# Kernel tuning notes

Measured on AMD Instinct MI355X. Metric: run time of the kernel, lower is better.

The kernel has to match this reference:

```python
import jax, jax.numpy as jnp
import numpy as np

B, S, DK = 32, 2048, 64

def setup_inputs() -> dict:
    key = jax.random.key(0)
    kq, kk, kv = jax.random.split(key, 3)
    Q = jax.random.normal(kq, (B, S, DK), dtype=jnp.float32)
    K = jax.random.normal(kk, (B, S, DK), dtype=jnp.float32)
    V = jax.random.normal(kv, (B, S, DK), dtype=jnp.float32)
    return {"Q": Q, "K": K, "V": V}

def reference(Q, K, V):
    # attn_scores = Q K^T / sqrt(d_k); full [B,S,S] probs materialized (naive, non-flash)
    d_k = Q.shape[-1]
    scores = jnp.einsum('bqd,bkd->bqk', Q, K) / jnp.sqrt(jnp.asarray(d_k, Q.dtype))
    probs = jax.nn.softmax(scores, axis=-1)
    return jnp.einsum('bqk,bkd->bqd', probs, V)
```

## Files before the change

### kernel.cpp

```cpp
#include <hip/hip_runtime.h>
#include <hip/hip_bf16.h>

#define BATCH 32
#define SEQ   2048
#define DKK   64

constexpr int QT  = 128;
constexpr int KT  = 64;
constexpr int NIT = SEQ / KT;
constexpr int LST = 66;

typedef __attribute__((ext_vector_type(8)))  short bf16x8;
typedef __attribute__((ext_vector_type(16))) float f32x16;
typedef __attribute__((ext_vector_type(2)))  unsigned uint2v;

__device__ __forceinline__ unsigned cvt2(float a, float b) {
    union { __hip_bfloat162 h; unsigned u; } c;
    c.h = __float22bfloat162_rn(make_float2(a, b));
    return c.u;
}

__device__ __forceinline__ float fast_exp2(float x) {
#if __has_builtin(__builtin_amdgcn_exp2f)
    return __builtin_amdgcn_exp2f(x);
#else
    return exp2f(x);
#endif
}

__global__ __launch_bounds__(256, 2) void attn_fwd(
        const float* __restrict__ Q, const float* __restrict__ K,
        const float* __restrict__ V, float* __restrict__ O) {
    __shared__ short Kb[2][KT][LST];
    __shared__ short Vt[2][DKK][LST];

    const int tid  = threadIdx.x;
    const int w    = tid >> 6;
    const int lane = tid & 63;
    const int hi   = lane >> 5;
    const int l31  = lane & 31;

    const int lin  = (int)blockIdx.x + ((int)blockIdx.y << 4);
    const int work = ((lin & 7) << 6) | (lin >> 3);
    const int b    = work >> 4;
    const int q0   = (work & 15) * QT + w * 32;

    const float qscale = 0.125f * 1.44269504088896340736f;
    bf16x8 qfrag[4];
    #pragma unroll
    for (int c = 0; c < 4; ++c) {
        const float* qp = Q + ((size_t)b * SEQ + q0 + l31) * DKK + 16*c + 8*hi;
        float4 a  = *(const float4*)qp;
        float4 a2 = *(const float4*)(qp + 4);
        union { bf16x8 v; unsigned u[4]; } f;
        f.u[0] = cvt2(a.x*qscale,  a.y*qscale);
        f.u[1] = cvt2(a.z*qscale,  a.w*qscale);
        f.u[2] = cvt2(a2.x*qscale, a2.y*qscale);
        f.u[3] = cvt2(a2.z*qscale, a2.w*qscale);
        qfrag[c] = f.v;
    }

    f32x16 o0 = {}, o1 = {};
    float lsum = 0.f;

    const float* Kbase = K + (size_t)b * SEQ * DKK;
    const float* Vbase = V + (size_t)b * SEQ * DKK;

    const int krow0 = tid >> 4;
    const int kcol  = (tid & 15) << 2;
    const int vd    = tid & 63;
    const int vg    = (tid >> 6) << 4;

    float4 kp[4];
    float  vp[16];
    auto load_regs = [&](int t) {
        const float* Kg = Kbase + (size_t)(t * KT) * DKK;
        #pragma unroll
        for (int i = 0; i < 4; ++i)
            kp[i] = *(const float4*)(Kg + (size_t)(krow0 + 16*i) * DKK + kcol);
        const float* Vg = Vbase + (size_t)(t * KT + vg) * DKK + vd;
        #pragma unroll
        for (int i = 0; i < 16; ++i) vp[i] = Vg[(size_t)i * DKK];
    };
    auto write_lds = [&](int buf) {
        #pragma unroll
        for (int i = 0; i < 4; ++i) {
            int2 kk;
            kk.x = (int)cvt2(kp[i].x, kp[i].y);
            kk.y = (int)cvt2(kp[i].z, kp[i].w);
            *(int2*)&Kb[buf][krow0 + 16*i][kcol] = kk;
        }
        union { bf16x8 v; unsigned u[4]; } t0, t1;
        t0.u[0] = cvt2(vp[0],  vp[1]);  t0.u[1] = cvt2(vp[2],  vp[3]);
        t0.u[2] = cvt2(vp[4],  vp[5]);  t0.u[3] = cvt2(vp[6],  vp[7]);
        t1.u[0] = cvt2(vp[8],  vp[9]);  t1.u[1] = cvt2(vp[10], vp[11]);
        t1.u[2] = cvt2(vp[12], vp[13]); t1.u[3] = cvt2(vp[14], vp[15]);
        *(bf16x8*)&Vt[buf][vd][vg]     = t0.v;
        *(bf16x8*)&Vt[buf][vd][vg + 8] = t1.v;
    };

    load_regs(0);
    write_lds(0);
    load_regs(1);
    __syncthreads();

    for (int it = 0; it < NIT; ++it) {
        const int cur = it & 1;

        #pragma unroll
        for (int kt2 = 0; kt2 < 2; ++kt2) {
            f32x16 acc = {};
            #pragma unroll
            for (int c = 0; c < 4; ++c) {
                bf16x8 kf = *(const bf16x8*)&Kb[cur][32*kt2 + l31][16*c + 8*hi];
                acc = __builtin_amdgcn_mfma_f32_32x32x16_bf16(kf, qfrag[c], acc, 0, 0, 0);
            }
            float p[16];
            #pragma unroll
            for (int r = 0; r < 16; ++r) { p[r] = fast_exp2(acc[r]); lsum += p[r]; }

            unsigned pw0 = cvt2(p[0],  p[1]),  pw1 = cvt2(p[2],  p[3]);
            unsigned pw2 = cvt2(p[4],  p[5]),  pw3 = cvt2(p[6],  p[7]);
            unsigned pw4 = cvt2(p[8],  p[9]),  pw5 = cvt2(p[10], p[11]);
            unsigned pw6 = cvt2(p[12], p[13]), pw7 = cvt2(p[14], p[15]);
            uint2v s02 = __builtin_amdgcn_permlane32_swap(pw0, pw2, false, false);
            uint2v s13 = __builtin_amdgcn_permlane32_swap(pw1, pw3, false, false);
            uint2v s46 = __builtin_amdgcn_permlane32_swap(pw4, pw6, false, false);
            uint2v s57 = __builtin_amdgcn_permlane32_swap(pw5, pw7, false, false);
            union { bf16x8 v; unsigned u[4]; } pa0, pa1;
            pa0.u[0] = s02[0]; pa0.u[1] = s13[0]; pa0.u[2] = s02[1]; pa0.u[3] = s13[1];
            pa1.u[0] = s46[0]; pa1.u[1] = s57[0]; pa1.u[2] = s46[1]; pa1.u[3] = s57[1];

            #pragma unroll
            for (int cc = 0; cc < 2; ++cc) {
                const int c = 2*kt2 + cc;
                bf16x8 pf  = cc ? pa1.v : pa0.v;
                bf16x8 vf0 = *(const bf16x8*)&Vt[cur][l31     ][16*c + 8*hi];
                bf16x8 vf1 = *(const bf16x8*)&Vt[cur][32 + l31][16*c + 8*hi];
                o0 = __builtin_amdgcn_mfma_f32_32x32x16_bf16(vf0, pf, o0, 0, 0, 0);
                o1 = __builtin_amdgcn_mfma_f32_32x32x16_bf16(vf1, pf, o1, 0, 0, 0);
            }
        }

        if (it + 1 < NIT) {
            write_lds(1 - cur);
            if (it + 2 < NIT) load_regs(it + 2);
            __syncthreads();
        }
    }

    float s = lsum;
    s += __shfl_xor(s, 32);
    const float inv = 1.0f / s;

    float* op = O + ((size_t)b * SEQ + q0 + l31) * DKK;
    #pragma unroll
    for (int G = 0; G < 4; ++G) {
        float4 st;
        st.x = o0[4*G + 0] * inv; st.y = o0[4*G + 1] * inv;
        st.z = o0[4*G + 2] * inv; st.w = o0[4*G + 3] * inv;
        *(float4*)(op + 8*G + 4*hi) = st;
        st.x = o1[4*G + 0] * inv; st.y = o1[4*G + 1] * inv;
        st.z = o1[4*G + 2] * inv; st.w = o1[4*G + 3] * inv;
        *(float4*)(op + 32 + 8*G + 4*hi) = st;
    }
}

extern "C" void kernel_launch(void* const* d_in, const int* in_sizes, int n_in,
                              void* d_out, int out_size, void* d_ws, size_t ws_size,
                              hipStream_t stream) {
    const float* Q = (const float*)d_in[0];
    const float* K = (const float*)d_in[1];
    const float* V = (const float*)d_in[2];
    float* O = (float*)d_out;
    dim3 grid(SEQ / QT, BATCH);
    attn_fwd<<<grid, dim3(256), 0, stream>>>(Q, K, V, O);
}
```

Measured before the change: 135.8 us.

## Process two query subtiles per wave with 128-thread blocks

Halves the block to two waves, each computing 64 query rows as two 32-row subtiles that share every K and V fragment read from LDS. Each thread loads and converts twice as much K/V per tile. MFMA sections are wrapped in s_setprio, and the sync becomes an explicit lgkmcnt wait plus raw barrier. This aims to cut LDS traffic per MFMA, at the cost of higher register pressure and fewer waves for latency hiding.

New measurement: 214.8 us. +58.1%, slower.

```diff
diff --git a/kernel.cpp b/kernel.cpp
--- a/kernel.cpp
+++ b/kernel.cpp
@@ -28,7 +28,7 @@
 #endif
 }
 
-__global__ __launch_bounds__(256, 2) void attn_fwd(
+__global__ __launch_bounds__(128, 2) void attn_fwd(
         const float* __restrict__ Q, const float* __restrict__ K,
         const float* __restrict__ V, float* __restrict__ O) {
     __shared__ short Kb[2][KT][LST];
@@ -43,25 +43,28 @@
     const int lin  = (int)blockIdx.x + ((int)blockIdx.y << 4);
     const int work = ((lin & 7) << 6) | (lin >> 3);
     const int b    = work >> 4;
-    const int q0   = (work & 15) * QT + w * 32;
+    const int qw   = (work & 15) * QT + w * 64;
 
     const float qscale = 0.125f * 1.44269504088896340736f;
-    bf16x8 qfrag[4];
+    bf16x8 qfrag[2][4];
     #pragma unroll
-    for (int c = 0; c < 4; ++c) {
-        const float* qp = Q + ((size_t)b * SEQ + q0 + l31) * DKK + 16*c + 8*hi;
-        float4 a  = *(const float4*)qp;
-        float4 a2 = *(const float4*)(qp + 4);
-        union { bf16x8 v; unsigned u[4]; } f;
-        f.u[0] = cvt2(a.x*qscale,  a.y*qscale);
-        f.u[1] = cvt2(a.z*qscale,  a.w*qscale);
-        f.u[2] = cvt2(a2.x*qscale, a2.y*qscale);
-        f.u[3] = cvt2(a2.z*qscale, a2.w*qscale);
-        qfrag[c] = f.v;
-    }
-
-    f32x16 o0 = {}, o1 = {};
-    float lsum = 0.f;
+    for (int qh = 0; qh < 2; ++qh) {
+        #pragma unroll
+        for (int c = 0; c < 4; ++c) {
+            const float* qp = Q + ((size_t)b * SEQ + qw + 32*qh + l31) * DKK + 16*c + 8*hi;
+            float4 a  = *(const float4*)qp;
+            float4 a2 = *(const float4*)(qp + 4);
+            union { bf16x8 v; unsigned u[4]; } f;
+            f.u[0] = cvt2(a.x*qscale,  a.y*qscale);
+            f.u[1] = cvt2(a.z*qscale,  a.w*qscale);
+            f.u[2] = cvt2(a2.x*qscale, a2.y*qscale);
+            f.u[3] = cvt2(a2.z*qscale, a2.w*qscale);
+            qfrag[qh][c] = f.v;
+        }
+    }
+
+    f32x16 o00 = {}, o01 = {}, o10 = {}, o11 = {};
+    float lsumA = 0.f, lsumB = 0.f;
 
     const float* Kbase = K + (size_t)b * SEQ * DKK;
     const float* Vbase = V + (size_t)b * SEQ * DKK;
@@ -69,34 +72,43 @@
     const int krow0 = tid >> 4;
     const int kcol  = (tid & 15) << 2;
     const int vd    = tid & 63;
-    const int vg    = (tid >> 6) << 4;
-
-    float4 kp[4];
-    float  vp[16];
+    const int vh    = tid >> 6;
+
+    float4 kp[8];
+    float  vp[32];
     auto load_regs = [&](int t) {
         const float* Kg = Kbase + (size_t)(t * KT) * DKK;
         #pragma unroll
-        for (int i = 0; i < 4; ++i)
-            kp[i] = *(const float4*)(Kg + (size_t)(krow0 + 16*i) * DKK + kcol);
-        const float* Vg = Vbase + (size_t)(t * KT + vg) * DKK + vd;
-        #pragma unroll
-        for (int i = 0; i < 16; ++i) vp[i] = Vg[(size_t)i * DKK];
+        for (int i = 0; i < 8; ++i)
+            kp[i] = *(const float4*)(Kg + (size_t)(krow0 + 8*i) * DKK + kcol);
+        const float* Vg = Vbase + (size_t)(t * KT + 16*vh) * DKK + vd;
+        #pragma unroll
+        for (int i = 0; i < 16; ++i) vp[i]      = Vg[(size_t)i * DKK];
+        const float* Vg2 = Vg + (size_t)32 * DKK;
+        #pragma unroll
+        for (int i = 0; i < 16; ++i) vp[16 + i] = Vg2[(size_t)i * DKK];
     };
     auto write_lds = [&](int buf) {
         #pragma unroll
-        for (int i = 0; i < 4; ++i) {
+        for (int i = 0; i < 8; ++i) {
             int2 kk;
             kk.x = (int)cvt2(kp[i].x, kp[i].y);
             kk.y = (int)cvt2(kp[i].z, kp[i].w);
-            *(int2*)&Kb[buf][krow0 + 16*i][kcol] = kk;
-        }
-        union { bf16x8 v; unsigned u[4]; } t0, t1;
+            *(int2*)&Kb[buf][krow0 + 8*i][kcol] = kk;
+        }
+        union { bf16x8 v; unsigned u[4]; } t0, t1, t2, t3;
         t0.u[0] = cvt2(vp[0],  vp[1]);  t0.u[1] = cvt2(vp[2],  vp[3]);
         t0.u[2] = cvt2(vp[4],  vp[5]);  t0.u[3] = cvt2(vp[6],  vp[7]);
         t1.u[0] = cvt2(vp[8],  vp[9]);  t1.u[1] = cvt2(vp[10], vp[11]);
         t1.u[2] = cvt2(vp[12], vp[13]); t1.u[3] = cvt2(vp[14], vp[15]);
-        *(bf16x8*)&Vt[buf][vd][vg]     = t0.v;
-        *(bf16x8*)&Vt[buf][vd][vg + 8] = t1.v;
+        t2.u[0] = cvt2(vp[16], vp[17]); t2.u[1] = cvt2(vp[18], vp[19]);
+        t2.u[2] = cvt2(vp[20], vp[21]); t2.u[3] = cvt2(vp[22], vp[23]);
+        t3.u[0] = cvt2(vp[24], vp[25]); t3.u[1] = cvt2(vp[26], vp[27]);
+        t3.u[2] = cvt2(vp[28], vp[29]); t3.u[3] = cvt2(vp[30], vp[31]);
+        *(bf16x8*)&Vt[buf][vd][16*vh]          = t0.v;
+        *(bf16x8*)&Vt[buf][vd][16*vh + 8]      = t1.v;
+        *(bf16x8*)&Vt[buf][vd][32 + 16*vh]     = t2.v;
+        *(bf16x8*)&Vt[buf][vd][32 + 16*vh + 8] = t3.v;
     };
 
     load_regs(0);
@@ -109,60 +121,104 @@
 
         #pragma unroll
         for (int kt2 = 0; kt2 < 2; ++kt2) {
-            f32x16 acc = {};
+            f32x16 aA = {}, aB = {};
+            __builtin_amdgcn_s_setprio(1);
             #pragma unroll
             for (int c = 0; c < 4; ++c) {
                 bf16x8 kf = *(const bf16x8*)&Kb[cur][32*kt2 + l31][16*c + 8*hi];
-                acc = __builtin_amdgcn_mfma_f32_32x32x16_bf16(kf, qfrag[c], acc, 0, 0, 0);
-            }
-            float p[16];
-            #pragma unroll
-            for (int r = 0; r < 16; ++r) { p[r] = fast_exp2(acc[r]); lsum += p[r]; }
-
-            unsigned pw0 = cvt2(p[0],  p[1]),  pw1 = cvt2(p[2],  p[3]);
-            unsigned pw2 = cvt2(p[4],  p[5]),  pw3 = cvt2(p[6],  p[7]);
-            unsigned pw4 = cvt2(p[8],  p[9]),  pw5 = cvt2(p[10], p[11]);
-            unsigned pw6 = cvt2(p[12], p[13]), pw7 = cvt2(p[14], p[15]);
-            uint2v s02 = __builtin_amdgcn_permlane32_swap(pw0, pw2, false, false);
-            uint2v s13 = __builtin_amdgcn_permlane32_swap(pw1, pw3, false, false);
-            uint2v s46 = __builtin_amdgcn_permlane32_swap(pw4, pw6, false, false);
-            uint2v s57 = __builtin_amdgcn_permlane32_swap(pw5, pw7, false, false);
-            union { bf16x8 v; unsigned u[4]; } pa0, pa1;
-            pa0.u[0] = s02[0]; pa0.u[1] = s13[0]; pa0.u[2] = s02[1]; pa0.u[3] = s13[1];
-            pa1.u[0] = s46[0]; pa1.u[1] = s57[0]; pa1.u[2] = s46[1]; pa1.u[3] = s57[1];
-
+                aA = __builtin_amdgcn_mfma_f32_32x32x16_bf16(kf, qfrag[0][c], aA, 0, 0, 0);
+                aB = __builtin_amdgcn_mfma_f32_32x32x16_bf16(kf, qfrag[1][c], aB, 0, 0, 0);
+            }
+            __builtin_amdgcn_s_setprio(0);
+
+            bf16x8 paA[2], paB[2];
+            {
+                float p[16];
+                #pragma unroll
+                for (int r = 0; r < 16; ++r) { p[r] = fast_exp2(aA[r]); lsumA += p[r]; }
+                unsigned pw0 = cvt2(p[0],  p[1]),  pw1 = cvt2(p[2],  p[3]);
+                unsigned pw2 = cvt2(p[4],  p[5]),  pw3 = cvt2(p[6],  p[7]);
+                unsigned pw4 = cvt2(p[8],  p[9]),  pw5 = cvt2(p[10], p[11]);
+                unsigned pw6 = cvt2(p[12], p[13]), pw7 = cvt2(p[14], p[15]);
+                uint2v s02 = __builtin_amdgcn_permlane32_swap(pw0, pw2, false, false);
+                uint2v s13 = __builtin_amdgcn_permlane32_swap(pw1, pw3, false, false);
+                uint2v s46 = __builtin_amdgcn_permlane32_swap(pw4, pw6, false, false);
+                uint2v s57 = __builtin_amdgcn_permlane32_swap(pw5, pw7, false, false);
+                union { bf16x8 v; unsigned u[4]; } pa0, pa1;
+                pa0.u[0] = s02[0]; pa0.u[1] = s13[0]; pa0.u[2] = s02[1]; pa0.u[3] = s13[1];
+                pa1.u[0] = s46[0]; pa1.u[1] = s57[0]; pa1.u[2] = s46[1]; pa1.u[3] = s57[1];
+                paA[0] = pa0.v; paA[1] = pa1.v;
+            }
+            {
+                float p[16];
+                #pragma unroll
+                for (int r = 0; r < 16; ++r) { p[r] = fast_exp2(aB[r]); lsumB += p[r]; }
+                unsigned pw0 = cvt2(p[0],  p[1]),  pw1 = cvt2(p[2],  p[3]);
+                unsigned pw2 = cvt2(p[4],  p[5]),  pw3 = cvt2(p[6],  p[7]);
+                unsigned pw4 = cvt2(p[8],  p[9]),  pw5 = cvt2(p[10], p[11]);
+                unsigned pw6 = cvt2(p[12], p[13]), pw7 = cvt2(p[14], p[15]);
+                uint2v s02 = __builtin_amdgcn_permlane32_swap(pw0, pw2, false, false);
+                uint2v s13 = __builtin_amdgcn_permlane32_swap(pw1, pw3, false, false);
+                uint2v s46 = __builtin_amdgcn_permlane32_swap(pw4, pw6, false, false);
+                uint2v s57 = __builtin_amdgcn_permlane32_swap(pw5, pw7, false, false);
+                union { bf16x8 v; unsigned u[4]; } pa0, pa1;
+                pa0.u[0] = s02[0]; pa0.u[1] = s13[0]; pa0.u[2] = s02[1]; pa0.u[3] = s13[1];
+                pa1.u[0] = s46[0]; pa1.u[1] = s57[0]; pa1.u[2] = s46[1]; pa1.u[3] = s57[1];
+                paB[0] = pa0.v; paB[1] = pa1.v;
+            }
+
+            __builtin_amdgcn_s_setprio(1);
             #pragma unroll
             for (int cc = 0; cc < 2; ++cc) {
                 const int c = 2*kt2 + cc;
-                bf16x8 pf  = cc ? pa1.v : pa0.v;
                 bf16x8 vf0 = *(const bf16x8*)&Vt[cur][l31     ][16*c + 8*hi];
                 bf16x8 vf1 = *(const bf16x8*)&Vt[cur][32 + l31][16*c + 8*hi];
-                o0 = __builtin_amdgcn_mfma_f32_32x32x16_bf16(vf0, pf, o0, 0, 0, 0);
-                o1 = __builtin_amdgcn_mfma_f32_32x32x16_bf16(vf1, pf, o1, 0, 0, 0);
-            }
+                o00 = __builtin_amdgcn_mfma_f32_32x32x16_bf16(vf0, paA[cc], o00, 0, 0, 0);
+                o01 = __builtin_amdgcn_mfma_f32_32x32x16_bf16(vf1, paA[cc], o01, 0, 0, 0);
+                o10 = __builtin_amdgcn_mfma_f32_32x32x16_bf16(vf0, paB[cc], o10, 0, 0, 0);
+                o11 = __builtin_amdgcn_mfma_f32_32x32x16_bf16(vf1, paB[cc], o11, 0, 0, 0);
+            }
+            __builtin_amdgcn_s_setprio(0);
         }
 
         if (it + 1 < NIT) {
             write_lds(1 - cur);
             if (it + 2 < NIT) load_regs(it + 2);
-            __syncthreads();
-        }
-    }
-
-    float s = lsum;
-    s += __shfl_xor(s, 32);
-    const float inv = 1.0f / s;
-
-    float* op = O + ((size_t)b * SEQ + q0 + l31) * DKK;
-    #pragma unroll
-    for (int G = 0; G < 4; ++G) {
-        float4 st;
-        st.x = o0[4*G + 0] * inv; st.y = o0[4*G + 1] * inv;
-        st.z = o0[4*G + 2] * inv; st.w = o0[4*G + 3] * inv;
-        *(float4*)(op + 8*G + 4*hi) = st;
-        st.x = o1[4*G + 0] * inv; st.y = o1[4*G + 1] * inv;
-        st.z = o1[4*G + 2] * inv; st.w = o1[4*G + 3] * inv;
-        *(float4*)(op + 32 + 8*G + 4*hi) = st;
+            asm volatile("s_waitcnt lgkmcnt(0)" ::: "memory");
+            __builtin_amdgcn_sched_barrier(0);
+            __builtin_amdgcn_s_barrier();
+            __builtin_amdgcn_sched_barrier(0);
+        }
+    }
+
+    float sA = lsumA; sA += __shfl_xor(sA, 32); const float invA = 1.0f / sA;
+    float sB = lsumB; sB += __shfl_xor(sB, 32); const float invB = 1.0f / sB;
+
+    {
+        float* op = O + ((size_t)b * SEQ + qw + l31) * DKK;
+        #pragma unroll
+        for (int G = 0; G < 4; ++G) {
+            float4 st;
+            st.x = o00[4*G + 0] * invA; st.y = o00[4*G + 1] * invA;
+            st.z = o00[4*G + 2] * invA; st.w = o00[4*G + 3] * invA;
+            *(float4*)(op + 8*G + 4*hi) = st;
+            st.x = o01[4*G + 0] * invA; st.y = o01[4*G + 1] * invA;
+            st.z = o01[4*G + 2] * invA; st.w = o01[4*G + 3] * invA;
+            *(float4*)(op + 32 + 8*G + 4*hi) = st;
+        }
+    }
+    {
+        float* op = O + ((size_t)b * SEQ + qw + 32 + l31) * DKK;
+        #pragma unroll
+        for (int G = 0; G < 4; ++G) {
+            float4 st;
+            st.x = o10[4*G + 0] * invB; st.y = o10[4*G + 1] * invB;
+            st.z = o10[4*G + 2] * invB; st.w = o10[4*G + 3] * invB;
+            *(float4*)(op + 8*G + 4*hi) = st;
+            st.x = o11[4*G + 0] * invB; st.y = o11[4*G + 1] * invB;
+            st.z = o11[4*G + 2] * invB; st.w = o11[4*G + 3] * invB;
+            *(float4*)(op + 32 + 8*G + 4*hi) = st;
+        }
     }
 }
 
@@ -174,5 +230,5 @@
     const float* V = (const float*)d_in[2];
     float* O = (float*)d_out;
     dim3 grid(SEQ / QT, BATCH);
-    attn_fwd<<<grid, dim3(256), 0, stream>>>(Q, K, V, O);
-}
+    attn_fwd<<<grid, dim3(128), 0, stream>>>(Q, K, V, O);
+}
```
